# Kernel optimization log

Hardware: AMD Instinct MI355X
Metric: run time of the kernel (lower is better)

## Reference

```python
import jax, jax.numpy as jnp
import numpy as np

NUM_TREES = 100
TREE_DEPTH = 5
INPUT_DIM = 256
NUM_CLASSES = 64
BATCH = 8192
NUM_NODES = 2 ** TREE_DEPTH - 1   # 31 decision nodes per tree
NUM_LEAVES = 2 ** TREE_DEPTH      # 32 leaves per tree


def setup_inputs() -> dict:
    key = jax.random.key(0)
    k_x, k_w, k_b, k_l = jax.random.split(key, 4)
    x = jax.random.normal(k_x, (BATCH, INPUT_DIM), dtype=jnp.float32)
    # stacked per-tree decision-node params (torch.randn init)
    node_w = jax.random.normal(k_w, (NUM_TREES, NUM_NODES, INPUT_DIM), dtype=jnp.float32)
    node_b = jax.random.normal(k_b, (NUM_TREES, NUM_NODES), dtype=jnp.float32)
    leaves = jax.random.normal(k_l, (NUM_TREES, NUM_LEAVES, NUM_CLASSES), dtype=jnp.float32)
    return {"x": x, "node_w": node_w, "node_b": node_b, "leaves": leaves}


def reference(x, node_w, node_b, leaves):
    # x: [B, D]; node_w: [T, Nn, D]; node_b: [T, Nn]; leaves: [T, Nl, C]
    T = node_w.shape[0]
    B = x.shape[0]
    depth = int(np.log2(leaves.shape[1]))
    idx = jnp.zeros((T, B), dtype=jnp.int32)
    for _ in range(depth):  # small fixed depth loop
        # gather each sample's routing node per tree: [T, B, D] and [T, B]
        w_g = jnp.take_along_axis(node_w, idx[:, :, None], axis=1)
        b_g = jnp.take_along_axis(node_b, idx, axis=1)
        decisions = jax.nn.sigmoid(jnp.einsum('tbd,bd->tb', w_g, x) + b_g)
        idx = 2 * idx + (decisions <= 0.5).astype(jnp.int32)
    # leaf gather: [T, B, C], then forest average over trees -> [B, C]
    tree_preds = jnp.take_along_axis(leaves, idx[:, :, None], axis=1)
    return jnp.mean(tree_preds, axis=0)
```

## Files before the change

### kernel.cpp

```cpp
#include <hip/hip_runtime.h>


typedef __bf16 bf16;
typedef __attribute__((ext_vector_type(8))) __bf16 bf16x8;
typedef __attribute__((ext_vector_type(4))) float f32x4;

#define NTREES 100
#define NB     8192
#define ND     256
#define NNODES 31
#define NLEAF  32
#define NCLS   64
#define TAU    2.0e-3f
#define FQCAP  32

__global__ void prep(const float* __restrict__ x, const float* __restrict__ wf,
                     const float* __restrict__ lv,
                     bf16* __restrict__ xh, bf16* __restrict__ xl,
                     bf16* __restrict__ wimg, bf16* __restrict__ lv16) {
    if (blockIdx.x < 1024) {
        int i = blockIdx.x * 256 + threadIdx.x;
        int m  = i & 15;
        int dq = (i >> 4) & 31;
        int g  = i >> 9;
        const float* src = x + (size_t)(g * 16 + m) * ND + dq * 8;
        bf16x8 h8, l8;
#pragma unroll
        for (int e = 0; e < 8; ++e) {
            float f = src[e];
            bf16 h = (bf16)f;
            h8[e] = h;
            l8[e] = (bf16)(f - (float)h);
        }
        *(bf16x8*)(xh + (size_t)i * 8) = h8;
        *(bf16x8*)(xl + (size_t)i * 8) = l8;
    } else if (blockIdx.x < 1224) {
        int i = (blockIdx.x - 1024) * 256 + threadIdx.x;
        int oct = i & 31;
        int row = (i >> 5) & 63;
        int tg  = i >> 11;
        int tree = tg * 4 + (row >> 4), node = row & 15;
        const float* src = wf + ((size_t)tree * NNODES + node) * ND + oct * 8;
        bf16x8 h8, l8;
#pragma unroll
        for (int e = 0; e < 8; ++e) {
            float f = src[e];
            bf16 h = (bf16)f;
            h8[e] = h;
            l8[e] = (bf16)(f - (float)h);
        }
        int kc = oct >> 4, c = oct & 15, cp = c ^ (row & 7);
        size_t b = (size_t)tg * 32768 + (size_t)kc * 16384 + row * 128 + cp * 8;
        *(bf16x8*)(wimg + b)        = h8;
        *(bf16x8*)(wimg + b + 8192) = l8;
    } else {
        int i = (blockIdx.x - 1224) * 256 + threadIdx.x;
        lv16[i] = (bf16)lv[i];
    }
}

__global__ __launch_bounds__(256, 4) void forest_all(
    const bf16* __restrict__ xh, const bf16* __restrict__ xl,
    const bf16* __restrict__ wimg,
    const float* __restrict__ x,
    const float* __restrict__ wf,
    const float* __restrict__ bias,
    unsigned char* __restrict__ idxb)
{
    __shared__ char lds[32768];
    __shared__ int fcnt;
    __shared__ unsigned short fitems[FQCAP];
    __shared__ unsigned char  fres[FQCAP];
    bf16*  Wh  = (bf16*)lds;
    bf16*  Wl  = (bf16*)(lds + 16384);
    float* scr = (float*)lds;

    const int tid  = threadIdx.x;
    const int wave = tid >> 6;
    const int lane = tid & 63;
    const int m    = lane & 15;
    const int q    = lane >> 4;

    const int lin  = blockIdx.x + gridDim.x * blockIdx.y;
    const int xcd  = lin & 7;
    const int slot = lin >> 3;
    const int mg   = xcd * 4 + (slot / 25);
    const int tg   = slot % 25;

    if (tid == 0) fcnt = 0;

    float biasv[4];
#pragma unroll
    for (int ni = 0; ni < 4; ++ni)
        biasv[ni] = bias[(size_t)(tg * 4 + ni) * NNODES + m];

    f32x4 acc[4][4];
#pragma unroll
    for (int mi = 0; mi < 4; ++mi)
#pragma unroll
        for (int ni = 0; ni < 4; ++ni)
            acc[mi][ni] = (f32x4){0.f, 0.f, 0.f, 0.f};

    size_t abase[4];
#pragma unroll
    for (int mi = 0; mi < 4; ++mi)
        abase[mi] = (size_t)(mg * 16 + wave * 4 + mi) * 4096 + lane * 8;

    const bf16* wsrc = wimg + (size_t)tg * 32768;

#pragma unroll
    for (int kc = 0; kc < 2; ++kc) {
        __syncthreads();
#pragma unroll
        for (int j = 0; j < 8; ++j) {
            int idx = j * 256 + tid;
            *(bf16x8*)(lds + idx * 16) =
                *(const bf16x8*)(wsrc + (size_t)kc * 16384 + idx * 8);
        }
        __syncthreads();

#pragma unroll
        for (int kk = 0; kk < 4; ++kk) {
            bf16x8 ah[4], al[4];
#pragma unroll
            for (int mi = 0; mi < 4; ++mi) {
                size_t off = abase[mi] + (size_t)(kc * 16 + kk * 4) * 128;
                ah[mi] = *(const bf16x8*)(xh + off);
                al[mi] = *(const bf16x8*)(xl + off);
            }
#pragma unroll
            for (int ni = 0; ni < 4; ++ni) {
                const int n    = ni * 16 + m;
                const int cidx = (4 * kk + q) ^ (m & 7);
                bf16x8 bh = *(const bf16x8*)(Wh + n * 128 + cidx * 8);
                bf16x8 bl = *(const bf16x8*)(Wl + n * 128 + cidx * 8);
#pragma unroll
                for (int mi = 0; mi < 4; ++mi) {
                    acc[mi][ni] = __builtin_amdgcn_mfma_f32_16x16x32_bf16(al[mi], bh, acc[mi][ni], 0, 0, 0);
                    acc[mi][ni] = __builtin_amdgcn_mfma_f32_16x16x32_bf16(ah[mi], bl, acc[mi][ni], 0, 0, 0);
                    acc[mi][ni] = __builtin_amdgcn_mfma_f32_16x16x32_bf16(ah[mi], bh, acc[mi][ni], 0, 0, 0);
                }
            }
        }
    }
    __syncthreads();

    float* ws_ = scr + wave * 1088;
    const int s_l = wave * 64 + lane;
    const int sg  = mg * 256 + s_l;
    unsigned int pk = 0;
#pragma unroll
    for (int ni = 0; ni < 4; ++ni) {
#pragma unroll
        for (int mi = 0; mi < 4; ++mi)
#pragma unroll
            for (int r = 0; r < 4; ++r)
                ws_[(mi * 16 + q * 4 + r) * 17 + m] = acc[mi][ni][r] + biasv[ni];
        int node = 0;
        float mn = 1e30f;
#pragma unroll
        for (int lvl = 0; lvl < 5; ++lvl) {
            float z = ws_[lane * 17 + node];
            mn = fminf(mn, fabsf(z));
            node = 2 * node + (z <= 0.0f ? 1 : 0);
        }
        pk |= (unsigned)node << (8 * ni);
        if (mn < TAU) {
            int p = atomicAdd(&fcnt, 1);
            if (p < FQCAP) fitems[p] = (unsigned short)((s_l << 2) | ni);
        }
    }
    __syncthreads();

    int cnt = fcnt;
    if (cnt > FQCAP) cnt = FQCAP;
    for (int i = wave; i < cnt; i += 4) {
        int it  = fitems[i];
        int sl2 = it >> 2, ni = it & 3;
        int t   = tg * 4 + ni;
        const float* xr = x + (size_t)(mg * 256 + sl2) * ND;
        float4 xv = *(const float4*)(xr + lane * 4);
        int node = 0;
        for (int lvl = 0; lvl < 5; ++lvl) {
            const float* wr = wf + ((size_t)t * NNODES + node) * ND;
            float4 wv = *(const float4*)(wr + lane * 4);
            double zz = (double)xv.x * wv.x + (double)xv.y * wv.y
                      + (double)xv.z * wv.z + (double)xv.w * wv.w;
#pragma unroll
            for (int o = 32; o > 0; o >>= 1) zz += __shfl_xor(zz, o);
            zz += (double)bias[t * NNODES + node];
            node = 2 * node + (zz <= 0.0 ? 1 : 0);
        }
        if (lane == 0) fres[i] = (unsigned char)node;
    }
    __syncthreads();

    for (int i = 0; i < cnt; ++i) {
        int it = fitems[i];
        if ((it >> 2) == s_l) {
            int ni = it & 3;
            pk = (pk & ~(255u << (8 * ni))) | ((unsigned)fres[i] << (8 * ni));
        }
    }
    *(unsigned int*)(idxb + (size_t)sg * NTREES + tg * 4) = pk;
}

__global__ void leaf_gather(const unsigned char* __restrict__ idxb,
                            const bf16* __restrict__ lv16,
                            float* __restrict__ out) {
    const int wave = threadIdx.x >> 6;
    const int lane = threadIdx.x & 63;
    const int s = blockIdx.x * 4 + wave;
    unsigned int rw = 0;
    if (lane < 25) rw = *(const unsigned int*)(idxb + (size_t)s * NTREES + lane * 4);
    float acc = 0.f;
#pragma unroll 10
    for (int t = 0; t < NTREES; ++t) {
        unsigned int wrd = __shfl(rw, t >> 2);
        int li = (wrd >> ((t & 3) * 8)) & 255;
        acc += (float)lv16[((size_t)t * NLEAF + li) * NCLS + lane];
    }
    out[(size_t)s * NCLS + lane] = acc * 0.01f;
}

extern "C" void kernel_launch(void* const* d_in, const int* in_sizes, int n_in,
                              void* d_out, int out_size, void* d_ws, size_t ws_size,
                              hipStream_t stream) {
    const float* x  = (const float*)d_in[0];
    const float* nw = (const float*)d_in[1];
    const float* nb = (const float*)d_in[2];
    const float* lv = (const float*)d_in[3];
    float* out = (float*)d_out;

    char* ws = (char*)d_ws;
    bf16* xh   = (bf16*)(ws + 0);
    bf16* xl   = (bf16*)(ws + 4194304);
    bf16* wimg = (bf16*)(ws + 8388608);
    unsigned char* idxb = (unsigned char*)(ws + 10027008);
    bf16* lv16 = (bf16*)(ws + 10846208);
    if (ws_size < (size_t)11255808) return;

    prep<<<2024, 256, 0, stream>>>(x, nw, lv, xh, xl, wimg, lv16);
    forest_all<<<dim3(25, 32), 256, 0, stream>>>(
        xh, xl, wimg, x, nw, nb, idxb);
    leaf_gather<<<NB / 4, 256, 0, stream>>>(idxb, lv16, out);
}
```

Measured before the change: 118.9 us.

## Move fp64 fixup to separate kernel, async LDS weight loads, prefetch A fragments

Result: faster. 110.2 us (-7.3%).

```diff
diff --git a/kernel.cpp b/kernel.cpp
--- a/kernel.cpp
+++ b/kernel.cpp
@@ -12,12 +12,20 @@
 #define NLEAF  32
 #define NCLS   64
 #define TAU    2.0e-3f
-#define FQCAP  32
+#define QCAP   8192
+
+static __device__ __forceinline__ void gload16(const void* g, void* l) {
+    __builtin_amdgcn_global_load_lds(
+        (const __attribute__((address_space(1))) void*)g,
+        (__attribute__((address_space(3))) void*)l, 16, 0, 0);
+}
 
 __global__ void prep(const float* __restrict__ x, const float* __restrict__ wf,
                      const float* __restrict__ lv,
                      bf16* __restrict__ xh, bf16* __restrict__ xl,
-                     bf16* __restrict__ wimg, bf16* __restrict__ lv16) {
+                     bf16* __restrict__ wimg, bf16* __restrict__ lv16,
+                     unsigned int* __restrict__ qcount) {
+    if (blockIdx.x == 0 && threadIdx.x == 0) *qcount = 0;
     if (blockIdx.x < 1024) {
         int i = blockIdx.x * 256 + threadIdx.x;
         int m  = i & 15;
@@ -59,18 +67,14 @@
     }
 }
 
-__global__ __launch_bounds__(256, 4) void forest_all(
+__global__ __launch_bounds__(256, 3) void forest_all(
     const bf16* __restrict__ xh, const bf16* __restrict__ xl,
     const bf16* __restrict__ wimg,
-    const float* __restrict__ x,
-    const float* __restrict__ wf,
     const float* __restrict__ bias,
-    unsigned char* __restrict__ idxb)
+    unsigned char* __restrict__ idxb,
+    unsigned int* __restrict__ qcount, unsigned int* __restrict__ queue)
 {
     __shared__ char lds[32768];
-    __shared__ int fcnt;
-    __shared__ unsigned short fitems[FQCAP];
-    __shared__ unsigned char  fres[FQCAP];
     bf16*  Wh  = (bf16*)lds;
     bf16*  Wl  = (bf16*)(lds + 16384);
     float* scr = (float*)lds;
@@ -87,8 +91,6 @@
     const int mg   = xcd * 4 + (slot / 25);
     const int tg   = slot % 25;
 
-    if (tid == 0) fcnt = 0;
-
     float biasv[4];
 #pragma unroll
     for (int ni = 0; ni < 4; ++ni)
@@ -108,25 +110,33 @@
 
     const bf16* wsrc = wimg + (size_t)tg * 32768;
 
+    bf16x8 cah[4], cal[4], nah[4], nal[4];
+#pragma unroll
+    for (int mi = 0; mi < 4; ++mi) {
+        cah[mi] = *(const bf16x8*)(xh + abase[mi]);
+        cal[mi] = *(const bf16x8*)(xl + abase[mi]);
+    }
+
 #pragma unroll
     for (int kc = 0; kc < 2; ++kc) {
         __syncthreads();
 #pragma unroll
         for (int j = 0; j < 8; ++j) {
             int idx = j * 256 + tid;
-            *(bf16x8*)(lds + idx * 16) =
-                *(const bf16x8*)(wsrc + (size_t)kc * 16384 + idx * 8);
+            gload16(wsrc + (size_t)kc * 16384 + idx * 8, lds + idx * 16);
         }
         __syncthreads();
 
 #pragma unroll
         for (int kk = 0; kk < 4; ++kk) {
-            bf16x8 ah[4], al[4];
-#pragma unroll
-            for (int mi = 0; mi < 4; ++mi) {
-                size_t off = abase[mi] + (size_t)(kc * 16 + kk * 4) * 128;
-                ah[mi] = *(const bf16x8*)(xh + off);
-                al[mi] = *(const bf16x8*)(xl + off);
+            if (kk < 3 || kc == 0) {
+                size_t step = (kk < 3) ? (size_t)(kc * 16 + (kk + 1) * 4) * 128
+                                       : (size_t)(16) * 128;
+#pragma unroll
+                for (int mi = 0; mi < 4; ++mi) {
+                    nah[mi] = *(const bf16x8*)(xh + abase[mi] + step);
+                    nal[mi] = *(const bf16x8*)(xl + abase[mi] + step);
+                }
             }
 #pragma unroll
             for (int ni = 0; ni < 4; ++ni) {
@@ -136,16 +146,18 @@
                 bf16x8 bl = *(const bf16x8*)(Wl + n * 128 + cidx * 8);
 #pragma unroll
                 for (int mi = 0; mi < 4; ++mi) {
-                    acc[mi][ni] = __builtin_amdgcn_mfma_f32_16x16x32_bf16(al[mi], bh, acc[mi][ni], 0, 0, 0);
-                    acc[mi][ni] = __builtin_amdgcn_mfma_f32_16x16x32_bf16(ah[mi], bl, acc[mi][ni], 0, 0, 0);
-                    acc[mi][ni] = __builtin_amdgcn_mfma_f32_16x16x32_bf16(ah[mi], bh, acc[mi][ni], 0, 0, 0);
+                    acc[mi][ni] = __builtin_amdgcn_mfma_f32_16x16x32_bf16(cal[mi], bh, acc[mi][ni], 0, 0, 0);
+                    acc[mi][ni] = __builtin_amdgcn_mfma_f32_16x16x32_bf16(cah[mi], bl, acc[mi][ni], 0, 0, 0);
+                    acc[mi][ni] = __builtin_amdgcn_mfma_f32_16x16x32_bf16(cah[mi], bh, acc[mi][ni], 0, 0, 0);
                 }
             }
+#pragma unroll
+            for (int mi = 0; mi < 4; ++mi) { cah[mi] = nah[mi]; cal[mi] = nal[mi]; }
         }
     }
     __syncthreads();
 
-    float* ws_ = scr + wave * 1088;
+    float* ws_ = scr + wave * 1280;
     const int s_l = wave * 64 + lane;
     const int sg  = mg * 256 + s_l;
     unsigned int pk = 0;
@@ -155,30 +167,61 @@
         for (int mi = 0; mi < 4; ++mi)
 #pragma unroll
             for (int r = 0; r < 4; ++r)
-                ws_[(mi * 16 + q * 4 + r) * 17 + m] = acc[mi][ni][r] + biasv[ni];
-        int node = 0;
-        float mn = 1e30f;
-#pragma unroll
-        for (int lvl = 0; lvl < 5; ++lvl) {
-            float z = ws_[lane * 17 + node];
-            mn = fminf(mn, fabsf(z));
-            node = 2 * node + (z <= 0.0f ? 1 : 0);
-        }
-        pk |= (unsigned)node << (8 * ni);
+                ws_[(mi * 16 + q * 4 + r) * 20 + m] = acc[mi][ni][r] + biasv[ni];
+        f32x4 z0 = *(f32x4*)&ws_[lane * 20];
+        f32x4 z1 = *(f32x4*)&ws_[lane * 20 + 4];
+        f32x4 z2 = *(f32x4*)&ws_[lane * 20 + 8];
+        f32x4 z3 = *(f32x4*)&ws_[lane * 20 + 12];
+        float z[16] = {z0[0], z0[1], z0[2], z0[3], z1[0], z1[1], z1[2], z1[3],
+                       z2[0], z2[1], z2[2], z2[3], z3[0], z3[1], z3[2], z3[3]};
+        float a0 = z[0];
+        bool d0 = a0 <= 0.f;
+        float a1 = d0 ? z[1] : z[0];
+        bool d1 = a1 <= 0.f;
+        float a2 = d0 ? (d1 ? z[3] : z[2]) : (d1 ? z[1] : z[0]);
+        bool d2 = a2 <= 0.f;
+        float m0 = d2 ? z[1] : z[0], m1 = d2 ? z[3] : z[2];
+        float m2 = d2 ? z[5] : z[4], m3 = d2 ? z[7] : z[6];
+        float p0 = d1 ? m1 : m0, p1 = d1 ? m3 : m2;
+        float a3 = d0 ? p1 : p0;
+        bool d3 = a3 <= 0.f;
+        float n0 = d3 ? z[1] : z[0],  n1 = d3 ? z[3] : z[2];
+        float n2 = d3 ? z[5] : z[4],  n3 = d3 ? z[7] : z[6];
+        float n4 = d3 ? z[9] : z[8],  n5 = d3 ? z[11] : z[10];
+        float n6 = d3 ? z[13] : z[12], n7 = d3 ? z[15] : z[14];
+        float q0 = d2 ? n1 : n0, q1 = d2 ? n3 : n2;
+        float q2 = d2 ? n5 : n4, q3 = d2 ? n7 : n6;
+        float r0 = d1 ? q1 : q0, r1 = d1 ? q3 : q2;
+        float a4 = d0 ? r1 : r0;
+        bool d4 = a4 <= 0.f;
+        int leaf = ((int)d0 << 4) | ((int)d1 << 3) | ((int)d2 << 2)
+                 | ((int)d3 << 1) | (int)d4;
+        pk |= (unsigned)leaf << (8 * ni);
+        float mn = fminf(fminf(fminf(fabsf(a0), fabsf(a1)),
+                               fminf(fabsf(a2), fabsf(a3))), fabsf(a4));
         if (mn < TAU) {
-            int p = atomicAdd(&fcnt, 1);
-            if (p < FQCAP) fitems[p] = (unsigned short)((s_l << 2) | ni);
-        }
-    }
-    __syncthreads();
-
-    int cnt = fcnt;
-    if (cnt > FQCAP) cnt = FQCAP;
-    for (int i = wave; i < cnt; i += 4) {
-        int it  = fitems[i];
-        int sl2 = it >> 2, ni = it & 3;
-        int t   = tg * 4 + ni;
-        const float* xr = x + (size_t)(mg * 256 + sl2) * ND;
+            unsigned int pos = atomicAdd(qcount, 1u);
+            if (pos < QCAP)
+                queue[pos] = ((unsigned)(tg * 4 + ni) << 13) | (unsigned)sg;
+        }
+        __syncthreads();
+    }
+    *(unsigned int*)(idxb + (size_t)sg * NTREES + tg * 4) = pk;
+}
+
+__global__ void fixup_kernel(const float* __restrict__ x, const float* __restrict__ wf,
+                             const float* __restrict__ bias,
+                             const unsigned int* __restrict__ qcount,
+                             const unsigned int* __restrict__ queue,
+                             unsigned char* __restrict__ idxb) {
+    const int wid  = (blockIdx.x * 256 + threadIdx.x) >> 6;
+    const int lane = threadIdx.x & 63;
+    unsigned int n = *qcount;
+    if (n > QCAP) n = QCAP;
+    for (unsigned int it = wid; it < n; it += 256) {
+        unsigned int e = queue[it];
+        int t = e >> 13, s = e & 8191;
+        const float* xr = x + (size_t)s * ND;
         float4 xv = *(const float4*)(xr + lane * 4);
         int node = 0;
         for (int lvl = 0; lvl < 5; ++lvl) {
@@ -191,18 +234,8 @@
             zz += (double)bias[t * NNODES + node];
             node = 2 * node + (zz <= 0.0 ? 1 : 0);
         }
-        if (lane == 0) fres[i] = (unsigned char)node;
-    }
-    __syncthreads();
-
-    for (int i = 0; i < cnt; ++i) {
-        int it = fitems[i];
-        if ((it >> 2) == s_l) {
-            int ni = it & 3;
-            pk = (pk & ~(255u << (8 * ni))) | ((unsigned)fres[i] << (8 * ni));
-        }
-    }
-    *(unsigned int*)(idxb + (size_t)sg * NTREES + tg * 4) = pk;
+        if (lane == 0) idxb[(size_t)s * NTREES + t] = (unsigned char)node;
+    }
 }
 
 __global__ void leaf_gather(const unsigned char* __restrict__ idxb,
@@ -238,10 +271,13 @@
     bf16* wimg = (bf16*)(ws + 8388608);
     unsigned char* idxb = (unsigned char*)(ws + 10027008);
     bf16* lv16 = (bf16*)(ws + 10846208);
-    if (ws_size < (size_t)11255808) return;
-
-    prep<<<2024, 256, 0, stream>>>(x, nw, lv, xh, xl, wimg, lv16);
+    unsigned int* qcount = (unsigned int*)(ws + 11255808);
+    unsigned int* queue  = (unsigned int*)(ws + 11255824);
+    if (ws_size < (size_t)11288592) return;
+
+    prep<<<2024, 256, 0, stream>>>(x, nw, lv, xh, xl, wimg, lv16, qcount);
     forest_all<<<dim3(25, 32), 256, 0, stream>>>(
-        xh, xl, wimg, x, nw, nb, idxb);
+        xh, xl, wimg, nb, idxb, qcount, queue);
+    fixup_kernel<<<64, 256, 0, stream>>>(x, nw, nb, qcount, queue, idxb);
     leaf_gather<<<NB / 4, 256, 0, stream>>>(idxb, lv16, out);
 }
```
